# Performance work log

Hardware: AMD Instinct MI355X
Metric: run time of the kernel (lower is better)

Reference implementation:

```python
import jax, jax.numpy as jnp
import numpy as np

B, C, H, W = 16, 64, 64, 64
MID = max(1, C // 8)


def setup_inputs() -> dict:
    key = jax.random.key(0)
    k1, k2, k3, k4, k5 = jax.random.split(key, 5)
    x = jax.random.normal(k1, (B, C, H, W), dtype=jnp.float32)
    # 1x1 conv weights (spectral-norm conv collapses to a plain [out,in] matrix
    # with a scalar-normalized weight; we use the effective weight directly)
    Wq = jax.random.normal(k2, (MID, C), dtype=jnp.float32) * 0.05
    Wk = jax.random.normal(k3, (MID, C), dtype=jnp.float32) * 0.05
    Wv = jax.random.normal(k4, (C, C), dtype=jnp.float32) * 0.05
    gamma = jax.random.normal(k5, (1,), dtype=jnp.float32) * 0.1
    return {"x": x, "Wq": Wq, "Wk": Wk, "Wv": Wv, "gamma": gamma}


def reference(x, Wq, Wk, Wv, gamma):
    b, c, h, w = x.shape
    n = h * w
    mid = Wq.shape[0]
    xf = x.reshape(b, c, n)                      # [B,C,N]
    q = jnp.einsum('mc,bcn->bnm', Wq, xf)        # [B,N,mid]
    k = jnp.einsum('mc,bcn->bmn', Wk, xf)        # [B,mid,N]
    scale = np.float32(1.0 / np.sqrt(mid))       # torch: / q.size(-1)**0.5, q last dim = mid
    attn = jax.nn.softmax(jnp.einsum('bnm,bmk->bnk', q, k) * scale, axis=-1)  # [B,N,N]
    v = jnp.einsum('oc,bcn->bon', Wv, xf)        # [B,C,N]
    # torch: bmm(v, attn^T) -> out[b,c,j] = sum_n v[b,c,n] * attn[b,j,n]
    out = jnp.einsum('bon,bjn->boj', v, attn).reshape(b, c, h, w)
    return gamma * out + x
```

## Files before the change

kernel.cpp:

```cpp
#include <hip/hip_runtime.h>
#include <hip/hip_bf16.h>

#define BATCH 16
#define CC    64
#define NN    4096
#define MIDD  8

typedef __attribute__((ext_vector_type(8)))  short short8;
typedef __attribute__((ext_vector_type(16))) float f32x16;
typedef __attribute__((ext_vector_type(2)))  int   v2i;

static __device__ __forceinline__ ushort f2bf(float f) {
    return __bfloat16_as_ushort(__float2bfloat16(f));
}

static __device__ __forceinline__ void glds16(const void* g, void* l) {
    __builtin_amdgcn_global_load_lds(
        (const __attribute__((address_space(1))) unsigned int*)g,
        (__attribute__((address_space(3))) unsigned int*)l, 16, 0, 0);
}

__global__ __launch_bounds__(256) void proj_kernel(
    const float* __restrict__ x,
    const float* __restrict__ Wq,
    const float* __restrict__ Wk,
    const float* __restrict__ Wv,
    ushort* __restrict__ qtr,
    ushort* __restrict__ ktr,
    ushort* __restrict__ v)
{
    __shared__ __align__(16) float sW[80 * 64];

    int tid = threadIdx.x;
    for (int i = tid; i < 512; i += 256) { sW[i] = Wq[i]; sW[512 + i] = Wk[i]; }
    for (int i = tid; i < 4096; i += 256) sW[1024 + i] = Wv[i];
    __syncthreads();

    int wv = tid >> 6;
    int nl = tid & 63;
    int g  = blockIdx.x * 64 + nl;
    int b  = g >> 12;
    int n  = g & (NN - 1);

    const float* xp = x + (size_t)b * CC * NN + n;
    const float* wb = sW + wv * 20 * 64;

    float acc[20];
#pragma unroll
    for (int i = 0; i < 20; ++i) acc[i] = 0.f;

#pragma unroll 1
    for (int cc = 0; cc < 64; cc += 16) {
        float xv[16];
#pragma unroll
        for (int i = 0; i < 16; ++i) xv[i] = xp[(size_t)(cc + i) * NN];

#pragma unroll
        for (int m = 0; m < 20; ++m) {
            const float4* w4 = (const float4*)(wb + m * 64 + cc);
            float4 w0 = w4[0], w1 = w4[1], w2 = w4[2], w3 = w4[3];
            float a = acc[m];
            a += w0.x * xv[0]  + w0.y * xv[1]  + w0.z * xv[2]  + w0.w * xv[3];
            a += w1.x * xv[4]  + w1.y * xv[5]  + w1.z * xv[6]  + w1.w * xv[7];
            a += w2.x * xv[8]  + w2.y * xv[9]  + w2.z * xv[10] + w2.w * xv[11];
            a += w3.x * xv[12] + w3.y * xv[13] + w3.z * xv[14] + w3.w * xv[15];
            acc[m] = a;
        }
    }

    const float SCLQ = 0.35355339059327373f * 1.4426950408889634f;
    if (wv == 0) {
        union { short8 s8; ushort us[8]; } qb;
#pragma unroll
        for (int m = 0; m < 8; ++m) qb.us[m] = f2bf(acc[m] * SCLQ);
        *(short8*)(qtr + ((size_t)b * NN + n) * 8) = qb.s8;

        union { uint4 u4[2]; ushort us[16]; } kb2;
#pragma unroll
        for (int m = 0; m < 8; ++m) kb2.us[m] = f2bf(acc[8 + m]);
#pragma unroll
        for (int m = 8; m < 16; ++m) kb2.us[m] = 0;
        ushort* kd = ktr + ((size_t)b * NN + n) * 16;
        *(uint4*)kd       = kb2.u4[0];
        *(uint4*)(kd + 8) = kb2.u4[1];
#pragma unroll
        for (int i = 0; i < 4; ++i)
            v[((size_t)b * CC + i) * NN + n] = f2bf(acc[16 + i]);
    } else {
        int rb = wv * 20 - 16;
#pragma unroll
        for (int i = 0; i < 20; ++i)
            v[((size_t)b * CC + rb + i) * NN + n] = f2bf(acc[i]);
    }
}

__global__ __launch_bounds__(256, 2) void attn_kernel(
    const ushort* __restrict__ qtr,
    const ushort* __restrict__ ktr,
    const ushort* __restrict__ v,
    const float*  __restrict__ x,
    const float*  __restrict__ gamma,
    float* __restrict__ out)
{
    __shared__ __align__(16) char lds[3 * 5120];

    int bid = blockIdx.x;
    int wg  = (bid & 7) * 64 + (bid >> 3);
    int b   = wg >> 5;
    int qt  = wg & 31;

    int tid  = threadIdx.x;
    int wv   = tid >> 6;
    int lane = tid & 63;
    int hi   = lane >> 5;
    int ql   = lane & 31;
    int q0   = qt * 128 + wv * 32;

    short8 qf = *(const short8*)(qtr + ((size_t)b * NN + q0 + ql) * 8);
    float  gm = gamma[0];
    short8 zero8 = {};
    if (hi) qf = zero8;
    asm volatile("s_waitcnt vmcnt(0)" ::: "memory");

    const ushort* kb_ = ktr + (size_t)b * NN * 16;
    const ushort* vb_ = v   + (size_t)b * CC * NN;

    int so   = tid >> 2;
    int slog = (tid & 3) ^ ((so >> 1) & 3);
    const ushort* vsrc0 = vb_ + (size_t)so * NN + slog * 8;
    const ushort* ksrc0 = kb_ + (size_t)(tid & 31) * 16 + (tid >> 5) * 8;
    int vdsto = tid * 16;
    int kdsto = 4096 + tid * 16;

    int x0  = (ql >> 1) & 3;
    int gA0 = (4 * ql + (hi ^ x0)) * 16;
    int gA1 = (4 * ql + ((2 + hi) ^ x0)) * 16;
    int gB0 = 2048 + gA0;
    int gB1 = 2048 + gA1;
    int koff = 4096 + (hi * 32 + ql) * 16;

    char* b0 = lds;
    char* b1 = lds + 5120;
    char* b2 = lds + 10240;

    union { short8 s8; ushort us[8]; } onesu;
#pragma unroll
    for (int i = 0; i < 8; ++i) onesu.us[i] = 0x3F80;
    short8 ones = onesu.s8;

    f32x16 zf   = {};
    f32x16 acc0 = {};
    f32x16 acc1 = {};
    f32x16 accl = {};

    glds16(vsrc0, b0 + vdsto);
    if (wv == 0) glds16(ksrc0, b0 + kdsto);
    glds16(vsrc0 + 32, b1 + vdsto);
    if (wv == 0) glds16(ksrc0 + 32 * 16, b1 + kdsto);

    for (int t = 0; t < 128; ++t) {
        int k2 = ((t + 2) & 127) * 32;

        __builtin_amdgcn_s_barrier();
        glds16(vsrc0 + k2, b2 + vdsto);
        if (wv == 0) {
            glds16(ksrc0 + (size_t)k2 * 16, b2 + kdsto);
            asm volatile("s_waitcnt vmcnt(4)" ::: "memory");
        } else {
            asm volatile("s_waitcnt vmcnt(2)" ::: "memory");
        }
        __builtin_amdgcn_s_barrier();
        __builtin_amdgcn_sched_barrier(0);

        short8 kfrag = *(const short8*)(b0 + koff);
        f32x16 s = __builtin_amdgcn_mfma_f32_32x32x16_bf16(kfrag, qf, zf, 0, 0, 0);

        float p[16];
#pragma unroll
        for (int r = 0; r < 16; ++r) p[r] = __builtin_amdgcn_exp2f(s[r]);

        unsigned u[8];
#pragma unroll
        for (int i = 0; i < 8; ++i)
            asm("v_cvt_pk_bf16_f32 %0, %1, %2"
                : "=v"(u[i]) : "v"(p[2 * i]), "v"(p[2 * i + 1]));

        v2i r02 = __builtin_amdgcn_permlane32_swap(u[0], u[2], false, false);
        v2i r13 = __builtin_amdgcn_permlane32_swap(u[1], u[3], false, false);
        v2i r46 = __builtin_amdgcn_permlane32_swap(u[4], u[6], false, false);
        v2i r57 = __builtin_amdgcn_permlane32_swap(u[5], u[7], false, false);
        union { short8 s8; int i4[4]; } P0, P1;
        P0.i4[0] = r02.x; P0.i4[1] = r13.x; P0.i4[2] = r02.y; P0.i4[3] = r13.y;
        P1.i4[0] = r46.x; P1.i4[1] = r57.x; P1.i4[2] = r46.y; P1.i4[3] = r57.y;

        short8 vaA0 = *(const short8*)(b0 + gA0);
        short8 vaA1 = *(const short8*)(b0 + gA1);
        short8 vaB0 = *(const short8*)(b0 + gB0);
        short8 vaB1 = *(const short8*)(b0 + gB1);

        __builtin_amdgcn_s_setprio(1);
        acc0 = __builtin_amdgcn_mfma_f32_32x32x16_bf16(vaA0, P0.s8, acc0, 0, 0, 0);
        acc1 = __builtin_amdgcn_mfma_f32_32x32x16_bf16(vaB0, P0.s8, acc1, 0, 0, 0);
        accl = __builtin_amdgcn_mfma_f32_32x32x16_bf16(ones, P0.s8, accl, 0, 0, 0);
        acc0 = __builtin_amdgcn_mfma_f32_32x32x16_bf16(vaA1, P1.s8, acc0, 0, 0, 0);
        acc1 = __builtin_amdgcn_mfma_f32_32x32x16_bf16(vaB1, P1.s8, acc1, 0, 0, 0);
        accl = __builtin_amdgcn_mfma_f32_32x32x16_bf16(ones, P1.s8, accl, 0, 0, 0);
        __builtin_amdgcn_s_setprio(0);

        char* tp = b0; b0 = b1; b1 = b2; b2 = tp;
    }

    float inv = gm / accl[0];

#pragma unroll
    for (int r = 0; r < 16; ++r) {
        int o = (r & 3) + 8 * (r >> 2) + 4 * hi;
        size_t i0 = ((size_t)(b * CC + o)) * NN + q0 + ql;
        out[i0] = acc0[r] * inv + x[i0];
        size_t i1 = i0 + (size_t)32 * NN;
        out[i1] = acc1[r] * inv + x[i1];
    }
}

extern "C" void kernel_launch(void* const* d_in, const int* in_sizes, int n_in,
                              void* d_out, int out_size, void* d_ws, size_t ws_size,
                              hipStream_t stream) {
    const float* x     = (const float*)d_in[0];
    const float* Wq    = (const float*)d_in[1];
    const float* Wk    = (const float*)d_in[2];
    const float* Wv    = (const float*)d_in[3];
    const float* gamma = (const float*)d_in[4];
    float* out = (float*)d_out;

    ushort* qtr = (ushort*)d_ws;
    ushort* ktr = qtr + (size_t)BATCH * NN * 8;
    ushort* vws = ktr + (size_t)BATCH * NN * 16;

    proj_kernel<<<dim3((BATCH * NN) / 64), dim3(256), 0, stream>>>(x, Wq, Wk, Wv, qtr, ktr, vws);
    attn_kernel<<<dim3((BATCH * NN) / 128), dim3(256), 0, stream>>>(qtr, ktr, vws, x, gamma, out);
}
```

Before: 158.2 us.

## Use MFMA for projections and double the attention key tile per barrier

The projection kernel now stages a bf16-transposed slice of x in LDS and computes the Q/K/V 1x1 convolutions with 32x32x16 bf16 MFMAs, with the weights held in registers, replacing the scalar FP32 FMA loops. The attention kernel processes 64 keys per pipeline stage instead of 32. This halves the number of loop iterations and barrier pairs, at the cost of double-sized LDS buffers and more registers for V fragments. Projection precision drops slightly because x and the weights are rounded to bf16 before the matmul.

```diff
diff --git a/kernel.cpp b/kernel.cpp
--- a/kernel.cpp
+++ b/kernel.cpp
@@ -18,6 +18,12 @@
     __builtin_amdgcn_global_load_lds(
         (const __attribute__((address_space(1))) unsigned int*)g,
         (__attribute__((address_space(3))) unsigned int*)l, 16, 0, 0);
+}
+
+static __device__ __forceinline__ unsigned cvt_pk(float lo, float hi) {
+    unsigned r;
+    asm("v_cvt_pk_bf16_f32 %0, %1, %2" : "=v"(r) : "v"(lo), "v"(hi));
+    return r;
 }
 
 __global__ __launch_bounds__(256) void proj_kernel(
@@ -29,68 +35,123 @@
     ushort* __restrict__ ktr,
     ushort* __restrict__ v)
 {
-    __shared__ __align__(16) float sW[80 * 64];
+    __shared__ unsigned xT[64 * 32];
 
     int tid = threadIdx.x;
-    for (int i = tid; i < 512; i += 256) { sW[i] = Wq[i]; sW[512 + i] = Wk[i]; }
-    for (int i = tid; i < 4096; i += 256) sW[1024 + i] = Wv[i];
+    int b   = blockIdx.x >> 6;
+    int n0  = (blockIdx.x & 63) * 64;
+
+    {
+        int n  = tid & 63;
+        int cp = tid >> 6;
+        const float* xb = x + (size_t)b * CC * NN + n0 + n;
+#pragma unroll
+        for (int rep = 0; rep < 8; ++rep) {
+            int c = cp * 2 + rep * 8;
+            float a0 = xb[(size_t)c * NN];
+            float a1 = xb[(size_t)(c + 1) * NN];
+            int dwlog = cp + rep * 4;
+            xT[n * 32 + (dwlog ^ (n & 31))] = cvt_pk(a0, a1);
+        }
+    }
+
+    int wv   = tid >> 6;
+    int lane = tid & 63;
+    int hi   = lane >> 5;
+    int r    = lane & 31;
+    int s_   = wv & 1;
+    bool hiT = wv >= 2;
+
+    short8 wfa[4], wfb[4];
+    if (!hiT) {
+        const float* r0 = (r < 8)  ? (Wq + r * 64)
+                        : (r < 16) ? (Wk + (r - 8) * 64)
+                                   : (Wv + (r - 16) * 64);
+        const float* r1 = Wv + (16 + r) * 64;
+#pragma unroll
+        for (int kc = 0; kc < 4; ++kc) {
+            const float4* p0 = (const float4*)(r0 + kc * 16 + hi * 8);
+            const float4* p1 = (const float4*)(r1 + kc * 16 + hi * 8);
+            float4 a = p0[0], c4 = p0[1];
+            float4 e = p1[0], g4 = p1[1];
+            union { short8 s8; unsigned u[4]; } wa, wb;
+            wa.u[0] = cvt_pk(a.x, a.y);  wa.u[1] = cvt_pk(a.z, a.w);
+            wa.u[2] = cvt_pk(c4.x, c4.y); wa.u[3] = cvt_pk(c4.z, c4.w);
+            wb.u[0] = cvt_pk(e.x, e.y);  wb.u[1] = cvt_pk(e.z, e.w);
+            wb.u[2] = cvt_pk(g4.x, g4.y); wb.u[3] = cvt_pk(g4.z, g4.w);
+            wfa[kc] = wa.s8; wfb[kc] = wb.s8;
+        }
+    } else {
+        const float* r2 = Wv + (size_t)(r < 16 ? (48 + r) : 48) * 64;
+        short8 z8 = {};
+#pragma unroll
+        for (int kc = 0; kc < 4; ++kc) {
+            const float4* p2 = (const float4*)(r2 + kc * 16 + hi * 8);
+            float4 a = p2[0], c4 = p2[1];
+            union { short8 s8; unsigned u[4]; } wa;
+            wa.u[0] = cvt_pk(a.x, a.y);  wa.u[1] = cvt_pk(a.z, a.w);
+            wa.u[2] = cvt_pk(c4.x, c4.y); wa.u[3] = cvt_pk(c4.z, c4.w);
+            wfa[kc] = (r < 16) ? wa.s8 : z8;
+            wfb[kc] = z8;
+        }
+    }
+
     __syncthreads();
 
-    int wv = tid >> 6;
-    int nl = tid & 63;
-    int g  = blockIdx.x * 64 + nl;
-    int b  = g >> 12;
-    int n  = g & (NN - 1);
-
-    const float* xp = x + (size_t)b * CC * NN + n;
-    const float* wb = sW + wv * 20 * 64;
-
-    float acc[20];
-#pragma unroll
-    for (int i = 0; i < 20; ++i) acc[i] = 0.f;
-
-#pragma unroll 1
-    for (int cc = 0; cc < 64; cc += 16) {
-        float xv[16];
-#pragma unroll
-        for (int i = 0; i < 16; ++i) xv[i] = xp[(size_t)(cc + i) * NN];
-
-#pragma unroll
-        for (int m = 0; m < 20; ++m) {
-            const float4* w4 = (const float4*)(wb + m * 64 + cc);
-            float4 w0 = w4[0], w1 = w4[1], w2 = w4[2], w3 = w4[3];
-            float a = acc[m];
-            a += w0.x * xv[0]  + w0.y * xv[1]  + w0.z * xv[2]  + w0.w * xv[3];
-            a += w1.x * xv[4]  + w1.y * xv[5]  + w1.z * xv[6]  + w1.w * xv[7];
-            a += w2.x * xv[8]  + w2.y * xv[9]  + w2.z * xv[10] + w2.w * xv[11];
-            a += w3.x * xv[12] + w3.y * xv[13] + w3.z * xv[14] + w3.w * xv[15];
-            acc[m] = a;
-        }
-    }
-
+    short8 bf[4];
+    int nr = s_ * 32 + r;
+#pragma unroll
+    for (int kc = 0; kc < 4; ++kc) {
+        union { short8 s8; unsigned u[4]; } bu;
+#pragma unroll
+        for (int i = 0; i < 4; ++i) {
+            int dwlog = kc * 8 + hi * 4 + i;
+            bu.u[i] = xT[nr * 32 + (dwlog ^ r)];
+        }
+        bf[kc] = bu.s8;
+    }
+
+    int ng = n0 + s_ * 32 + r;
+    size_t nb = (size_t)b * NN + ng;
     const float SCLQ = 0.35355339059327373f * 1.4426950408889634f;
-    if (wv == 0) {
-        union { short8 s8; ushort us[8]; } qb;
-#pragma unroll
-        for (int m = 0; m < 8; ++m) qb.us[m] = f2bf(acc[m] * SCLQ);
-        *(short8*)(qtr + ((size_t)b * NN + n) * 8) = qb.s8;
-
-        union { uint4 u4[2]; ushort us[16]; } kb2;
-#pragma unroll
-        for (int m = 0; m < 8; ++m) kb2.us[m] = f2bf(acc[8 + m]);
-#pragma unroll
-        for (int m = 8; m < 16; ++m) kb2.us[m] = 0;
-        ushort* kd = ktr + ((size_t)b * NN + n) * 16;
-        *(uint4*)kd       = kb2.u4[0];
-        *(uint4*)(kd + 8) = kb2.u4[1];
-#pragma unroll
-        for (int i = 0; i < 4; ++i)
-            v[((size_t)b * CC + i) * NN + n] = f2bf(acc[16 + i]);
+
+    if (!hiT) {
+        f32x16 acc = {};
+#pragma unroll
+        for (int kc = 0; kc < 4; ++kc)
+            acc = __builtin_amdgcn_mfma_f32_32x32x16_bf16(wfa[kc], bf[kc], acc, 0, 0, 0);
+        uint2 qd, kd, zd; zd.x = 0; zd.y = 0;
+        qd.x = cvt_pk(acc[0] * SCLQ, acc[1] * SCLQ);
+        qd.y = cvt_pk(acc[2] * SCLQ, acc[3] * SCLQ);
+        kd.x = cvt_pk(acc[4], acc[5]);
+        kd.y = cvt_pk(acc[6], acc[7]);
+        *(uint2*)(qtr + nb * 8 + hi * 4) = qd;
+        *(uint2*)(ktr + nb * 16 + hi * 4) = kd;
+        *(uint2*)(ktr + nb * 16 + 8 + hi * 4) = zd;
+#pragma unroll
+        for (int reg = 8; reg < 16; ++reg) {
+            int ch = (reg & 3) + 8 * ((reg >> 2) - 2) + 4 * hi;
+            v[((size_t)b * CC + ch) * NN + ng] = f2bf(acc[reg]);
+        }
+        f32x16 ac1 = {};
+#pragma unroll
+        for (int kc = 0; kc < 4; ++kc)
+            ac1 = __builtin_amdgcn_mfma_f32_32x32x16_bf16(wfb[kc], bf[kc], ac1, 0, 0, 0);
+#pragma unroll
+        for (int reg = 0; reg < 16; ++reg) {
+            int ch = 16 + (reg & 3) + 8 * (reg >> 2) + 4 * hi;
+            v[((size_t)b * CC + ch) * NN + ng] = f2bf(ac1[reg]);
+        }
     } else {
-        int rb = wv * 20 - 16;
-#pragma unroll
-        for (int i = 0; i < 20; ++i)
-            v[((size_t)b * CC + rb + i) * NN + n] = f2bf(acc[i]);
+        f32x16 acc = {};
+#pragma unroll
+        for (int kc = 0; kc < 4; ++kc)
+            acc = __builtin_amdgcn_mfma_f32_32x32x16_bf16(wfa[kc], bf[kc], acc, 0, 0, 0);
+#pragma unroll
+        for (int reg = 0; reg < 8; ++reg) {
+            int ch = 48 + (reg & 3) + 8 * (reg >> 2) + 4 * hi;
+            v[((size_t)b * CC + ch) * NN + ng] = f2bf(acc[reg]);
+        }
     }
 }
 
@@ -102,7 +163,7 @@
     const float*  __restrict__ gamma,
     float* __restrict__ out)
 {
-    __shared__ __align__(16) char lds[3 * 5120];
+    __shared__ __align__(16) char lds[3 * 10240];
 
     int bid = blockIdx.x;
     int wg  = (bid & 7) * 64 + (bid >> 3);
@@ -125,23 +186,16 @@
     const ushort* kb_ = ktr + (size_t)b * NN * 16;
     const ushort* vb_ = v   + (size_t)b * CC * NN;
 
-    int so   = tid >> 2;
-    int slog = (tid & 3) ^ ((so >> 1) & 3);
-    const ushort* vsrc0 = vb_ + (size_t)so * NN + slog * 8;
-    const ushort* ksrc0 = kb_ + (size_t)(tid & 31) * 16 + (tid >> 5) * 8;
-    int vdsto = tid * 16;
-    int kdsto = 4096 + tid * 16;
-
-    int x0  = (ql >> 1) & 3;
-    int gA0 = (4 * ql + (hi ^ x0)) * 16;
-    int gA1 = (4 * ql + ((2 + hi) ^ x0)) * 16;
-    int gB0 = 2048 + gA0;
-    int gB1 = 2048 + gA1;
-    int koff = 4096 + (hi * 32 + ql) * 16;
+    int oA = tid >> 3, sA = (tid & 7) ^ (oA & 7);
+    int oB = oA + 32,  sB = (tid & 7) ^ (oB & 7);
+    const ushort* vsrcA = vb_ + (size_t)oA * NN + sA * 8;
+    const ushort* vsrcB = vb_ + (size_t)oB * NN + sB * 8;
+    const ushort* ksrc0 = kb_ + (size_t)(tid & 63) * 16 + (tid >> 6) * 8;
+    int vdA = tid * 16, vdB = (tid + 256) * 16, kd_ = 8192 + tid * 16;
 
     char* b0 = lds;
-    char* b1 = lds + 5120;
-    char* b2 = lds + 10240;
+    char* b1 = lds + 10240;
+    char* b2 = lds + 20480;
 
     union { short8 s8; ushort us[8]; } onesu;
 #pragma unroll
@@ -153,59 +207,70 @@
     f32x16 acc1 = {};
     f32x16 accl = {};
 
-    glds16(vsrc0, b0 + vdsto);
-    if (wv == 0) glds16(ksrc0, b0 + kdsto);
-    glds16(vsrc0 + 32, b1 + vdsto);
-    if (wv == 0) glds16(ksrc0 + 32 * 16, b1 + kdsto);
-
-    for (int t = 0; t < 128; ++t) {
-        int k2 = ((t + 2) & 127) * 32;
+    glds16(vsrcA, b0 + vdA); glds16(vsrcB, b0 + vdB);
+    if (wv < 2) glds16(ksrc0, b0 + kd_);
+    glds16(vsrcA + 64, b1 + vdA); glds16(vsrcB + 64, b1 + vdB);
+    if (wv < 2) glds16(ksrc0 + 64 * 16, b1 + kd_);
+
+    for (int t = 0; t < 64; ++t) {
+        int k2 = ((t + 2) & 63) * 64;
 
         __builtin_amdgcn_s_barrier();
-        glds16(vsrc0 + k2, b2 + vdsto);
-        if (wv == 0) {
-            glds16(ksrc0 + (size_t)k2 * 16, b2 + kdsto);
+        glds16(vsrcA + k2, b2 + vdA);
+        glds16(vsrcB + k2, b2 + vdB);
+        if (wv < 2) {
+            glds16(ksrc0 + (size_t)k2 * 16, b2 + kd_);
+            asm volatile("s_waitcnt vmcnt(6)" ::: "memory");
+        } else {
             asm volatile("s_waitcnt vmcnt(4)" ::: "memory");
-        } else {
-            asm volatile("s_waitcnt vmcnt(2)" ::: "memory");
         }
         __builtin_amdgcn_s_barrier();
         __builtin_amdgcn_sched_barrier(0);
 
-        short8 kfrag = *(const short8*)(b0 + koff);
-        f32x16 s = __builtin_amdgcn_mfma_f32_32x32x16_bf16(kfrag, qf, zf, 0, 0, 0);
-
-        float p[16];
-#pragma unroll
-        for (int r = 0; r < 16; ++r) p[r] = __builtin_amdgcn_exp2f(s[r]);
-
-        unsigned u[8];
-#pragma unroll
-        for (int i = 0; i < 8; ++i)
-            asm("v_cvt_pk_bf16_f32 %0, %1, %2"
-                : "=v"(u[i]) : "v"(p[2 * i]), "v"(p[2 * i + 1]));
-
-        v2i r02 = __builtin_amdgcn_permlane32_swap(u[0], u[2], false, false);
-        v2i r13 = __builtin_amdgcn_permlane32_swap(u[1], u[3], false, false);
-        v2i r46 = __builtin_amdgcn_permlane32_swap(u[4], u[6], false, false);
-        v2i r57 = __builtin_amdgcn_permlane32_swap(u[5], u[7], false, false);
-        union { short8 s8; int i4[4]; } P0, P1;
-        P0.i4[0] = r02.x; P0.i4[1] = r13.x; P0.i4[2] = r02.y; P0.i4[3] = r13.y;
-        P1.i4[0] = r46.x; P1.i4[1] = r57.x; P1.i4[2] = r46.y; P1.i4[3] = r57.y;
-
-        short8 vaA0 = *(const short8*)(b0 + gA0);
-        short8 vaA1 = *(const short8*)(b0 + gA1);
-        short8 vaB0 = *(const short8*)(b0 + gB0);
-        short8 vaB1 = *(const short8*)(b0 + gB1);
-
-        __builtin_amdgcn_s_setprio(1);
-        acc0 = __builtin_amdgcn_mfma_f32_32x32x16_bf16(vaA0, P0.s8, acc0, 0, 0, 0);
-        acc1 = __builtin_amdgcn_mfma_f32_32x32x16_bf16(vaB0, P0.s8, acc1, 0, 0, 0);
-        accl = __builtin_amdgcn_mfma_f32_32x32x16_bf16(ones, P0.s8, accl, 0, 0, 0);
-        acc0 = __builtin_amdgcn_mfma_f32_32x32x16_bf16(vaA1, P1.s8, acc0, 0, 0, 0);
-        acc1 = __builtin_amdgcn_mfma_f32_32x32x16_bf16(vaB1, P1.s8, acc1, 0, 0, 0);
-        accl = __builtin_amdgcn_mfma_f32_32x32x16_bf16(ones, P1.s8, accl, 0, 0, 0);
-        __builtin_amdgcn_s_setprio(0);
+        short8 kf0 = *(const short8*)(b0 + 8192 + (hi * 64 + ql) * 16);
+        short8 kf1 = *(const short8*)(b0 + 8192 + (hi * 64 + 32 + ql) * 16);
+
+        short8 vA[2][2], vB[2][2];
+#pragma unroll
+        for (int c = 0; c < 2; ++c)
+#pragma unroll
+            for (int f = 0; f < 2; ++f) {
+                int byteA = (ql * 8 + ((c * 4 + f * 2 + hi) ^ (ql & 7))) * 16;
+                vA[c][f] = *(const short8*)(b0 + byteA);
+                vB[c][f] = *(const short8*)(b0 + byteA + 4096);
+            }
+
+        f32x16 s0 = __builtin_amdgcn_mfma_f32_32x32x16_bf16(kf0, qf, zf, 0, 0, 0);
+        f32x16 s1 = __builtin_amdgcn_mfma_f32_32x32x16_bf16(kf1, qf, zf, 0, 0, 0);
+
+#pragma unroll
+        for (int c = 0; c < 2; ++c) {
+            const f32x16& s = c ? s1 : s0;
+            float p[16];
+#pragma unroll
+            for (int r = 0; r < 16; ++r) p[r] = __builtin_amdgcn_exp2f(s[r]);
+
+            unsigned u[8];
+#pragma unroll
+            for (int i = 0; i < 8; ++i) u[i] = cvt_pk(p[2 * i], p[2 * i + 1]);
+
+            v2i r02 = __builtin_amdgcn_permlane32_swap(u[0], u[2], false, false);
+            v2i r13 = __builtin_amdgcn_permlane32_swap(u[1], u[3], false, false);
+            v2i r46 = __builtin_amdgcn_permlane32_swap(u[4], u[6], false, false);
+            v2i r57 = __builtin_amdgcn_permlane32_swap(u[5], u[7], false, false);
+            union { short8 s8; int i4[4]; } P0, P1;
+            P0.i4[0] = r02.x; P0.i4[1] = r13.x; P0.i4[2] = r02.y; P0.i4[3] = r13.y;
+            P1.i4[0] = r46.x; P1.i4[1] = r57.x; P1.i4[2] = r46.y; P1.i4[3] = r57.y;
+
+            __builtin_amdgcn_s_setprio(1);
+            acc0 = __builtin_amdgcn_mfma_f32_32x32x16_bf16(vA[c][0], P0.s8, acc0, 0, 0, 0);
+            acc1 = __builtin_amdgcn_mfma_f32_32x32x16_bf16(vB[c][0], P0.s8, acc1, 0, 0, 0);
+            accl = __builtin_amdgcn_mfma_f32_32x32x16_bf16(ones,    P0.s8, accl, 0, 0, 0);
+            acc0 = __builtin_amdgcn_mfma_f32_32x32x16_bf16(vA[c][1], P1.s8, acc0, 0, 0, 0);
+            acc1 = __builtin_amdgcn_mfma_f32_32x32x16_bf16(vB[c][1], P1.s8, acc1, 0, 0, 0);
+            accl = __builtin_amdgcn_mfma_f32_32x32x16_bf16(ones,    P1.s8, accl, 0, 0, 0);
+            __builtin_amdgcn_s_setprio(0);
+        }
 
         char* tp = b0; b0 = b1; b1 = b2; b2 = tp;
     }
```

New measurement: 144.3 us. 8.8% less time.
